# Performance work log

Measured on AMD Instinct MI355X. Metric: run time of the kernel, lower is better.

Reference implementation:

```python
import jax, jax.numpy as jnp
import numpy as np

DIM = 256
WH, WW = 7, 7
N = WH * WW
HEADS = 8
HEAD_DIM = DIM // HEADS
SCALE = HEAD_DIM ** -0.5
B_ = 4096
NW = 64  # windows per image; B_ % NW == 0


def _relative_position_index():
    coords = np.stack(np.meshgrid(np.arange(WH), np.arange(WW), indexing='ij'))  # (2,Wh,Ww)
    flat = coords.reshape(2, -1)  # (2,N)
    rel = flat[:, :, None] - flat[:, None, :]  # (2,N,N)
    rel = rel.transpose(1, 2, 0)  # (N,N,2)
    rel = rel + np.array([WH - 1, WW - 1])
    rel = rel * np.array([2 * WW - 1, 1])
    return rel.sum(-1).astype(np.int32)  # (N,N)


def setup_inputs() -> dict:
    key = jax.random.key(0)
    ks = jax.random.split(key, 7)
    num_rel = (2 * WH - 1) * (2 * WW - 1)
    return {
        'x': jax.random.normal(ks[0], (B_, N, DIM), jnp.float32),
        'mask': jax.random.normal(ks[1], (NW, N, N), jnp.float32),
        'qkv_w': jax.random.normal(ks[2], (DIM, 3 * DIM), jnp.float32) * 0.02,
        'qkv_b': jnp.zeros((3 * DIM,), jnp.float32),
        'proj_w': jax.random.normal(ks[3], (DIM, DIM), jnp.float32) * 0.02,
        'proj_b': jnp.zeros((DIM,), jnp.float32),
        'bias_table': jax.random.normal(ks[4], (num_rel, HEADS), jnp.float32) * 0.02,
        'rel_index': jnp.asarray(_relative_position_index()),
    }


def reference(x, mask, qkv_w, qkv_b, proj_w, proj_b, bias_table, rel_index):
    B, n, C = x.shape
    qkv = x @ qkv_w + qkv_b  # (B,N,3C)
    qkv = qkv.reshape(B, n, 3, HEADS, HEAD_DIM).transpose(2, 0, 3, 1, 4)
    q, k, v = qkv[0], qkv[1], qkv[2]  # (B,H,N,hd)
    attn = jnp.einsum('bhnd,bhmd->bhnm', q * SCALE, k)  # (B,H,N,N)
    rel_bias = bias_table[rel_index.reshape(-1)].reshape(n, n, HEADS)
    attn = attn + rel_bias.transpose(2, 0, 1)[None]  # (B,H,N,N)
    nW = mask.shape[0]
    attn = attn.reshape(-1, nW, HEADS, n, n) + mask[None, :, None]
    attn = attn.reshape(-1, HEADS, n, n)
    attn = jax.nn.softmax(attn, axis=-1)
    out = jnp.einsum('bhnm,bhmd->bhnd', attn, v)  # (B,H,N,hd)
    out = out.transpose(0, 2, 1, 3).reshape(B, n, C)
    return out @ proj_w + proj_b
```

## Files before the change

kernel.cpp:

```cpp
#include <hip/hip_runtime.h>
#include <hip/hip_bf16.h>


#define NTOK 49
static constexpr float SCALE_Q = 0.17677669529663687f;

using bf16   = __bf16;
using bf16x4 = __attribute__((ext_vector_type(4))) __bf16;
using bf16x8 = __attribute__((ext_vector_type(8))) __bf16;
using short4v = __attribute__((ext_vector_type(4))) short;
using f32x4  = __attribute__((ext_vector_type(4))) float;

#define WT_QKV_OFF 0
#define WT_PROJ_OFF (768 * 256 * 2)
#define SB_OFF (WT_PROJ_OFF + 256 * 256 * 2)
#define SM_OFF (SB_OFF + 8 * 4096 * 4)
#define WS_NEEDED (SM_OFF + (size_t)64 * 4096 * 4)

static __device__ __forceinline__ f32x4 mfma16(bf16x4 a, bf16x4 b, f32x4 c) {
#if __has_builtin(__builtin_amdgcn_mfma_f32_16x16x16_bf16)
    return __builtin_amdgcn_mfma_f32_16x16x16_bf16(a, b, c, 0, 0, 0);
#elif __has_builtin(__builtin_amdgcn_mfma_f32_16x16x16bf16_1k)
    return __builtin_amdgcn_mfma_f32_16x16x16bf16_1k(
        __builtin_bit_cast(short4v, a), __builtin_bit_cast(short4v, b), c, 0, 0, 0);
#elif __has_builtin(__builtin_amdgcn_mfma_f32_16x16x16_bf16_1k)
    return __builtin_amdgcn_mfma_f32_16x16x16_bf16_1k(
        __builtin_bit_cast(short4v, a), __builtin_bit_cast(short4v, b), c, 0, 0, 0);
#else
    asm volatile("v_mfma_f32_16x16x16_bf16 %0, %1, %2, %0\n\t"
                 "s_nop 7\n\ts_nop 7\n\ts_nop 1"
                 : "+v"(c) : "v"(a), "v"(b));
    return c;
#endif
}

__global__ void prep_wqkv(const float* __restrict__ qkv_w, bf16* __restrict__ wt) {
    int idx = blockIdx.x * 256 + threadIdx.x;
    if (idx >= 768 * 256) return;
    int n = idx >> 8, k = idx & 255;
    float v = qkv_w[k * 768 + n];
    if (n < 256) v *= SCALE_Q;
    wt[idx] = (bf16)v;
}
__global__ void prep_wproj(const float* __restrict__ proj_w, bf16* __restrict__ wt) {
    int idx = blockIdx.x * 256 + threadIdx.x;
    if (idx >= 256 * 256) return;
    int n = idx >> 8, k = idx & 255;
    wt[idx] = (bf16)proj_w[k * 256 + n];
}
__global__ void prep_sb(const float* __restrict__ bias_table, const int* __restrict__ rel_index,
                        float* __restrict__ sb) {
    int idx = blockIdx.x * 256 + threadIdx.x;
    if (idx >= 8 * 4096) return;
    int r    = idx & 3;
    int lane = (idx >> 2) & 63;
    int qp   = (idx >> 8) & 15;
    int h    = idx >> 12;
    int kt = qp >> 2, qt = qp & 3;
    int i = qt * 16 + (lane & 15);
    int j = kt * 16 + (lane >> 4) * 4 + r;
    float v;
    if (j >= NTOK)      v = -1e30f;
    else if (i >= NTOK) v = 0.0f;
    else v = bias_table[rel_index[i * 49 + j] * 8 + h];
    sb[idx] = v;
}
__global__ void prep_sm(const float* __restrict__ mask, float* __restrict__ sm) {
    int idx = blockIdx.x * 256 + threadIdx.x;
    if (idx >= 64 * 4096) return;
    int r    = idx & 3;
    int lane = (idx >> 2) & 63;
    int qp   = (idx >> 8) & 15;
    int w    = idx >> 12;
    int kt = qp >> 2, qt = qp & 3;
    int i = qt * 16 + (lane & 15);
    int j = kt * 16 + (lane >> 4) * 4 + r;
    sm[idx] = (i < NTOK && j < NTOK) ? mask[(w * 49 + i) * 49 + j] : 0.0f;
}

__global__ __launch_bounds__(512, 2) void fused_attn(
    const float* __restrict__ x,
    const float* __restrict__ qkv_b,
    const float* __restrict__ proj_b,
    const bf16* __restrict__ wt_qkv,
    const bf16* __restrict__ wt_proj,
    const float* __restrict__ sb,
    const float* __restrict__ sm,
    float* __restrict__ out)
{
    __shared__ char xs[32768];
    const int b    = blockIdx.x;
    const int tid  = threadIdx.x;
    const int lane = tid & 63;
    const int h    = tid >> 6;
    const int c    = lane & 15;
    const int g    = lane >> 4;

    {
        const float* xb = x + (size_t)b * (NTOK * 256);
        float4 xr[8];
        #pragma unroll
        for (int it = 0; it < 8; ++it) {
            int idx = it * 512 + tid;
            int row = idx >> 6, c4 = idx & 63;
            xr[it] = make_float4(0.f, 0.f, 0.f, 0.f);
            if (row < NTOK) xr[it] = ((const float4*)xb)[row * 64 + c4];
        }
        #pragma unroll
        for (int it = 0; it < 8; ++it) {
            int idx = it * 512 + tid;
            int row = idx >> 6, c4 = idx & 63;
            bf16x4 o;
            o[0] = (bf16)xr[it].x; o[1] = (bf16)xr[it].y;
            o[2] = (bf16)xr[it].z; o[3] = (bf16)xr[it].w;
            *(bf16x4*)(xs + row * 512 + ((c4 * 8) ^ ((row & 7) << 4))) = o;
        }
    }
    __syncthreads();

    bf16x4 iden;
    #pragma unroll
    for (int j = 0; j < 4; ++j) iden[j] = (bf16)((4 * g + j == c) ? 1.0f : 0.0f);

    bf16x4 qf[4][2];
    bf16x4 kf[4][2];
    bf16x4 pB[4][4];
    bf16x4 vf[2][4];
    bf16x4 ob[2][4];

    {
        f32x4 acc[2][4];
        #pragma unroll
        for (int ni = 0; ni < 2; ++ni)
            #pragma unroll
            for (int mi = 0; mi < 4; ++mi)
                acc[ni][mi] = (f32x4){0.f, 0.f, 0.f, 0.f};
        #pragma unroll
        for (int k2 = 0; k2 < 4; ++k2) {
            bf16x8 bb[2][2];
            #pragma unroll
            for (int ni = 0; ni < 2; ++ni)
                #pragma unroll
                for (int hf = 0; hf < 2; ++hf)
                    bb[ni][hf] = *(const bf16x8*)(wt_qkv + (h * 32 + ni * 16 + c) * 256
                                                  + k2 * 64 + hf * 32 + g * 8);
            bf16x8 a[2][4];
            #pragma unroll
            for (int hf = 0; hf < 2; ++hf)
                #pragma unroll
                for (int mi = 0; mi < 4; ++mi) {
                    int row = mi * 16 + c;
                    a[hf][mi] = *(const bf16x8*)(xs + row * 512
                                 + ((k2 * 128 + hf * 64 + g * 16) ^ ((row & 7) << 4)));
                }
            #pragma unroll
            for (int hf = 0; hf < 2; ++hf)
                #pragma unroll
                for (int ni = 0; ni < 2; ++ni)
                    #pragma unroll
                    for (int mi = 0; mi < 4; ++mi)
                        acc[ni][mi] = __builtin_amdgcn_mfma_f32_16x16x32_bf16(a[hf][mi], bb[ni][hf], acc[ni][mi], 0, 0, 0);
        }
        #pragma unroll
        for (int ni = 0; ni < 2; ++ni) {
            float bias = qkv_b[h * 32 + ni * 16 + c] * SCALE_Q;
            #pragma unroll
            for (int mi = 0; mi < 4; ++mi) {
                bf16x4 in;
                #pragma unroll
                for (int r = 0; r < 4; ++r) in[r] = (bf16)(acc[ni][mi][r] + bias);
                f32x4 t = mfma16(in, iden, (f32x4){0.f, 0.f, 0.f, 0.f});
                #pragma unroll
                for (int r = 0; r < 4; ++r) qf[mi][ni][r] = (bf16)t[r];
            }
        }
    }

    {
        f32x4 acc[2][4];
        #pragma unroll
        for (int ni = 0; ni < 2; ++ni)
            #pragma unroll
            for (int mi = 0; mi < 4; ++mi)
                acc[ni][mi] = (f32x4){0.f, 0.f, 0.f, 0.f};
        #pragma unroll
        for (int k2 = 0; k2 < 4; ++k2) {
            bf16x8 bb[2][2];
            #pragma unroll
            for (int ni = 0; ni < 2; ++ni)
                #pragma unroll
                for (int hf = 0; hf < 2; ++hf)
                    bb[ni][hf] = *(const bf16x8*)(wt_qkv + (256 + h * 32 + ni * 16 + c) * 256
                                                  + k2 * 64 + hf * 32 + g * 8);
            bf16x8 a[2][4];
            #pragma unroll
            for (int hf = 0; hf < 2; ++hf)
                #pragma unroll
                for (int mi = 0; mi < 4; ++mi) {
                    int row = mi * 16 + c;
                    a[hf][mi] = *(const bf16x8*)(xs + row * 512
                                 + ((k2 * 128 + hf * 64 + g * 16) ^ ((row & 7) << 4)));
                }
            #pragma unroll
            for (int hf = 0; hf < 2; ++hf)
                #pragma unroll
                for (int ni = 0; ni < 2; ++ni)
                    #pragma unroll
                    for (int mi = 0; mi < 4; ++mi)
                        acc[ni][mi] = __builtin_amdgcn_mfma_f32_16x16x32_bf16(a[hf][mi], bb[ni][hf], acc[ni][mi], 0, 0, 0);
        }
        #pragma unroll
        for (int ni = 0; ni < 2; ++ni) {
            float bias = qkv_b[256 + h * 32 + ni * 16 + c];
            #pragma unroll
            for (int mi = 0; mi < 4; ++mi) {
                bf16x4 in;
                #pragma unroll
                for (int r = 0; r < 4; ++r) in[r] = (bf16)(acc[ni][mi][r] + bias);
                f32x4 t = mfma16(in, iden, (f32x4){0.f, 0.f, 0.f, 0.f});
                #pragma unroll
                for (int r = 0; r < 4; ++r) kf[mi][ni][r] = (bf16)t[r];
            }
        }
    }

    {
        const float* sbh = sb + (size_t)h * 4096;
        const float* smw = sm + (size_t)(b & 63) * 4096;
        #pragma unroll
        for (int qt = 0; qt < 4; ++qt) {
            f32x4 sbv[4], smv[4];
            #pragma unroll
            for (int kt = 0; kt < 4; ++kt)
                sbv[kt] = *(const f32x4*)(sbh + (kt * 4 + qt) * 256 + lane * 4);
            #pragma unroll
            for (int kt = 0; kt < 4; ++kt)
                smv[kt] = *(const f32x4*)(smw + (kt * 4 + qt) * 256 + lane * 4);

            f32x4 sT[4];
            __builtin_amdgcn_s_setprio(1);
            #pragma unroll
            for (int kt = 0; kt < 4; ++kt) {
                sT[kt] = (f32x4){0.f, 0.f, 0.f, 0.f};
                sT[kt] = mfma16(kf[kt][0], qf[qt][0], sT[kt]);
                sT[kt] = mfma16(kf[kt][1], qf[qt][1], sT[kt]);
            }
            __builtin_amdgcn_s_setprio(0);
            #pragma unroll
            for (int kt = 0; kt < 4; ++kt)
                #pragma unroll
                for (int r = 0; r < 4; ++r)
                    sT[kt][r] += sbv[kt][r] + smv[kt][r];
            float m = sT[0][0];
            #pragma unroll
            for (int kt = 0; kt < 4; ++kt)
                #pragma unroll
                for (int r = 0; r < 4; ++r) m = fmaxf(m, sT[kt][r]);
            m = fmaxf(m, __shfl_xor(m, 16));
            m = fmaxf(m, __shfl_xor(m, 32));
            float sum = 0.f;
            #pragma unroll
            for (int kt = 0; kt < 4; ++kt)
                #pragma unroll
                for (int r = 0; r < 4; ++r) {
                    float e = __expf(sT[kt][r] - m);
                    sT[kt][r] = e;
                    sum += e;
                }
            sum += __shfl_xor(sum, 16);
            sum += __shfl_xor(sum, 32);
            float rs = 1.f / sum;
            #pragma unroll
            for (int kt = 0; kt < 4; ++kt)
                #pragma unroll
                for (int r = 0; r < 4; ++r) pB[qt][kt][r] = (bf16)(sT[kt][r] * rs);
        }
    }

    {
        f32x4 acc[2][4];
        #pragma unroll
        for (int dt = 0; dt < 2; ++dt)
            #pragma unroll
            for (int mi = 0; mi < 4; ++mi)
                acc[dt][mi] = (f32x4){0.f, 0.f, 0.f, 0.f};
        #pragma unroll
        for (int k2 = 0; k2 < 4; ++k2) {
            bf16x8 bb[2][2];
            #pragma unroll
            for (int dt = 0; dt < 2; ++dt)
                #pragma unroll
                for (int hf = 0; hf < 2; ++hf)
                    bb[dt][hf] = *(const bf16x8*)(wt_qkv + (512 + h * 32 + dt * 16 + c) * 256
                                                  + k2 * 64 + hf * 32 + g * 8);
            bf16x8 a[2][4];
            #pragma unroll
            for (int hf = 0; hf < 2; ++hf)
                #pragma unroll
                for (int mi = 0; mi < 4; ++mi) {
                    int row = mi * 16 + c;
                    a[hf][mi] = *(const bf16x8*)(xs + row * 512
                                 + ((k2 * 128 + hf * 64 + g * 16) ^ ((row & 7) << 4)));
                }
            #pragma unroll
            for (int hf = 0; hf < 2; ++hf)
                #pragma unroll
                for (int dt = 0; dt < 2; ++dt)
                    #pragma unroll
                    for (int mi = 0; mi < 4; ++mi)
                        acc[dt][mi] = __builtin_amdgcn_mfma_f32_16x16x32_bf16(a[hf][mi], bb[dt][hf], acc[dt][mi], 0, 0, 0);
        }
        #pragma unroll
        for (int dt = 0; dt < 2; ++dt) {
            float vb = qkv_b[512 + h * 32 + dt * 16 + c];
            #pragma unroll
            for (int kt = 0; kt < 4; ++kt)
                #pragma unroll
                for (int r = 0; r < 4; ++r) vf[dt][kt][r] = (bf16)(acc[dt][kt][r] + vb);
        }
    }

    __builtin_amdgcn_s_setprio(1);
    #pragma unroll
    for (int qt = 0; qt < 4; ++qt) {
        #pragma unroll
        for (int dt = 0; dt < 2; ++dt) {
            f32x4 oT = (f32x4){0.f, 0.f, 0.f, 0.f};
            #pragma unroll
            for (int kt = 0; kt < 4; ++kt)
                oT = mfma16(vf[dt][kt], pB[qt][kt], oT);
            #pragma unroll
            for (int r = 0; r < 4; ++r) ob[dt][qt][r] = (bf16)oT[r];
        }
    }
    __builtin_amdgcn_s_setprio(0);
    __syncthreads();

    #pragma unroll
    for (int qt = 0; qt < 4; ++qt) {
        int row = qt * 16 + c;
        #pragma unroll
        for (int dt = 0; dt < 2; ++dt) {
            int cbyte = h * 64 + dt * 32 + g * 8;
            *(bf16x4*)(xs + row * 512 + (cbyte ^ ((row & 7) << 4))) = ob[dt][qt];
        }
    }
    __syncthreads();

    {
        f32x4 po[2][4];
        #pragma unroll
        for (int ni = 0; ni < 2; ++ni)
            #pragma unroll
            for (int mi = 0; mi < 4; ++mi)
                po[ni][mi] = (f32x4){0.f, 0.f, 0.f, 0.f};

        #pragma unroll
        for (int k2 = 0; k2 < 4; ++k2) {
            bf16x8 bw[2][2];
            #pragma unroll
            for (int ni = 0; ni < 2; ++ni)
                #pragma unroll
                for (int hf = 0; hf < 2; ++hf)
                    bw[ni][hf] = *(const bf16x8*)(wt_proj + (h * 32 + ni * 16 + c) * 256
                                                  + k2 * 64 + hf * 32 + g * 8);
            bf16x8 a[2][4];
            #pragma unroll
            for (int hf = 0; hf < 2; ++hf)
                #pragma unroll
                for (int mi = 0; mi < 4; ++mi) {
                    int row = mi * 16 + c;
                    a[hf][mi] = *(const bf16x8*)(xs + row * 512
                                 + ((k2 * 128 + hf * 64 + g * 16) ^ ((row & 7) << 4)));
                }
            #pragma unroll
            for (int hf = 0; hf < 2; ++hf)
                #pragma unroll
                for (int ni = 0; ni < 2; ++ni)
                    #pragma unroll
                    for (int mi = 0; mi < 4; ++mi)
                        po[ni][mi] = __builtin_amdgcn_mfma_f32_16x16x32_bf16(a[hf][mi], bw[ni][hf], po[ni][mi], 0, 0, 0);
        }
        float* outb = out + (size_t)b * (NTOK * 256);
        #pragma unroll
        for (int ni = 0; ni < 2; ++ni) {
            int col = h * 32 + ni * 16 + c;
            float pb = proj_b[col];
            #pragma unroll
            for (int mi = 0; mi < 4; ++mi) {
                #pragma unroll
                for (int r = 0; r < 4; ++r) {
                    int row = mi * 16 + g * 4 + r;
                    if (row < NTOK) outb[row * 256 + col] = po[ni][mi][r] + pb;
                }
            }
        }
    }
}

extern "C" void kernel_launch(void* const* d_in, const int* in_sizes, int n_in,
                              void* d_out, int out_size, void* d_ws, size_t ws_size,
                              hipStream_t stream) {
    const float* x          = (const float*)d_in[0];
    const float* mask       = (const float*)d_in[1];
    const float* qkv_w      = (const float*)d_in[2];
    const float* qkv_b      = (const float*)d_in[3];
    const float* proj_w     = (const float*)d_in[4];
    const float* proj_b     = (const float*)d_in[5];
    const float* bias_table = (const float*)d_in[6];
    const int*   rel_index  = (const int*)d_in[7];
    float* out = (float*)d_out;

    if (ws_size < WS_NEEDED) return;

    char* ws = (char*)d_ws;
    bf16*  wt_qkv  = (bf16*)(ws + WT_QKV_OFF);
    bf16*  wt_proj = (bf16*)(ws + WT_PROJ_OFF);
    float* sbp     = (float*)(ws + SB_OFF);
    float* smp     = (float*)(ws + SM_OFF);

    prep_wqkv <<<768, 256, 0, stream>>>(qkv_w, wt_qkv);
    prep_wproj<<<256, 256, 0, stream>>>(proj_w, wt_proj);
    prep_sb   <<<128, 256, 0, stream>>>(bias_table, rel_index, sbp);
    prep_sm   <<<1024, 256, 0, stream>>>(mask, smp);

    fused_attn<<<4096, 512, 0, stream>>>(x, qkv_b, proj_b, wt_qkv, wt_proj, sbp, smp, out);
}
```

Measured before the change: 373.0 us.

## Cut register pressure to fit three blocks per CU in fused attention

Raises launch bounds from 2 to 3 blocks per multiprocessor and reshapes the QKV projection loops to load smaller register fragments per step (8 k-steps with 4 A-tiles instead of 4 with 8). The V projection is split per head-dim tile, the mask load is deferred until after the bias add, and the attention output is written straight to LDS instead of buffered in registers. The goal is to lower VGPR usage so more waves can overlap memory latency. The risk is register spilling under the tighter bound and fewer independent MFMAs in flight per step.

```diff
diff --git a/kernel.cpp b/kernel.cpp
--- a/kernel.cpp
+++ b/kernel.cpp
@@ -32,6 +32,10 @@
                  : "+v"(c) : "v"(a), "v"(b));
     return c;
 #endif
+}
+
+static __device__ __forceinline__ bf16x8 ldsA(const char* xs, int row, int koff) {
+    return *(const bf16x8*)(xs + row * 512 + (koff ^ ((row & 7) << 4)));
 }
 
 __global__ void prep_wqkv(const float* __restrict__ qkv_w, bf16* __restrict__ wt) {
@@ -78,7 +82,7 @@
     sm[idx] = (i < NTOK && j < NTOK) ? mask[(w * 49 + i) * 49 + j] : 0.0f;
 }
 
-__global__ __launch_bounds__(512, 2) void fused_attn(
+__global__ __launch_bounds__(512, 3) void fused_attn(
     const float* __restrict__ x,
     const float* __restrict__ qkv_b,
     const float* __restrict__ proj_b,
@@ -126,7 +130,6 @@
     bf16x4 kf[4][2];
     bf16x4 pB[4][4];
     bf16x4 vf[2][4];
-    bf16x4 ob[2][4];
 
     {
         f32x4 acc[2][4];
@@ -136,30 +139,20 @@
             for (int mi = 0; mi < 4; ++mi)
                 acc[ni][mi] = (f32x4){0.f, 0.f, 0.f, 0.f};
         #pragma unroll
-        for (int k2 = 0; k2 < 4; ++k2) {
-            bf16x8 bb[2][2];
-            #pragma unroll
-            for (int ni = 0; ni < 2; ++ni)
-                #pragma unroll
-                for (int hf = 0; hf < 2; ++hf)
-                    bb[ni][hf] = *(const bf16x8*)(wt_qkv + (h * 32 + ni * 16 + c) * 256
-                                                  + k2 * 64 + hf * 32 + g * 8);
-            bf16x8 a[2][4];
-            #pragma unroll
-            for (int hf = 0; hf < 2; ++hf)
-                #pragma unroll
-                for (int mi = 0; mi < 4; ++mi) {
-                    int row = mi * 16 + c;
-                    a[hf][mi] = *(const bf16x8*)(xs + row * 512
-                                 + ((k2 * 128 + hf * 64 + g * 16) ^ ((row & 7) << 4)));
-                }
-            #pragma unroll
-            for (int hf = 0; hf < 2; ++hf)
-                #pragma unroll
-                for (int ni = 0; ni < 2; ++ni)
-                    #pragma unroll
-                    for (int mi = 0; mi < 4; ++mi)
-                        acc[ni][mi] = __builtin_amdgcn_mfma_f32_16x16x32_bf16(a[hf][mi], bb[ni][hf], acc[ni][mi], 0, 0, 0);
+        for (int kk = 0; kk < 8; ++kk) {
+            bf16x8 bb[2];
+            #pragma unroll
+            for (int ni = 0; ni < 2; ++ni)
+                bb[ni] = *(const bf16x8*)(wt_qkv + (h * 32 + ni * 16 + c) * 256 + kk * 32 + g * 8);
+            bf16x8 a[4];
+            #pragma unroll
+            for (int mi = 0; mi < 4; ++mi)
+                a[mi] = ldsA(xs, mi * 16 + c, kk * 64 + g * 16);
+            #pragma unroll
+            for (int ni = 0; ni < 2; ++ni)
+                #pragma unroll
+                for (int mi = 0; mi < 4; ++mi)
+                    acc[ni][mi] = __builtin_amdgcn_mfma_f32_16x16x32_bf16(a[mi], bb[ni], acc[ni][mi], 0, 0, 0);
         }
         #pragma unroll
         for (int ni = 0; ni < 2; ++ni) {
@@ -184,30 +177,20 @@
             for (int mi = 0; mi < 4; ++mi)
                 acc[ni][mi] = (f32x4){0.f, 0.f, 0.f, 0.f};
         #pragma unroll
-        for (int k2 = 0; k2 < 4; ++k2) {
-            bf16x8 bb[2][2];
-            #pragma unroll
-            for (int ni = 0; ni < 2; ++ni)
-                #pragma unroll
-                for (int hf = 0; hf < 2; ++hf)
-                    bb[ni][hf] = *(const bf16x8*)(wt_qkv + (256 + h * 32 + ni * 16 + c) * 256
-                                                  + k2 * 64 + hf * 32 + g * 8);
-            bf16x8 a[2][4];
-            #pragma unroll
-            for (int hf = 0; hf < 2; ++hf)
-                #pragma unroll
-                for (int mi = 0; mi < 4; ++mi) {
-                    int row = mi * 16 + c;
-                    a[hf][mi] = *(const bf16x8*)(xs + row * 512
-                                 + ((k2 * 128 + hf * 64 + g * 16) ^ ((row & 7) << 4)));
-                }
-            #pragma unroll
-            for (int hf = 0; hf < 2; ++hf)
-                #pragma unroll
-                for (int ni = 0; ni < 2; ++ni)
-                    #pragma unroll
-                    for (int mi = 0; mi < 4; ++mi)
-                        acc[ni][mi] = __builtin_amdgcn_mfma_f32_16x16x32_bf16(a[hf][mi], bb[ni][hf], acc[ni][mi], 0, 0, 0);
+        for (int kk = 0; kk < 8; ++kk) {
+            bf16x8 bb[2];
+            #pragma unroll
+            for (int ni = 0; ni < 2; ++ni)
+                bb[ni] = *(const bf16x8*)(wt_qkv + (256 + h * 32 + ni * 16 + c) * 256 + kk * 32 + g * 8);
+            bf16x8 a[4];
+            #pragma unroll
+            for (int mi = 0; mi < 4; ++mi)
+                a[mi] = ldsA(xs, mi * 16 + c, kk * 64 + g * 16);
+            #pragma unroll
+            for (int ni = 0; ni < 2; ++ni)
+                #pragma unroll
+                for (int mi = 0; mi < 4; ++mi)
+                    acc[ni][mi] = __builtin_amdgcn_mfma_f32_16x16x32_bf16(a[mi], bb[ni], acc[ni][mi], 0, 0, 0);
         }
         #pragma unroll
         for (int ni = 0; ni < 2; ++ni) {
@@ -229,13 +212,10 @@
         const float* smw = sm + (size_t)(b & 63) * 4096;
         #pragma unroll
         for (int qt = 0; qt < 4; ++qt) {
-            f32x4 sbv[4], smv[4];
+            f32x4 sbv[4];
             #pragma unroll
             for (int kt = 0; kt < 4; ++kt)
                 sbv[kt] = *(const f32x4*)(sbh + (kt * 4 + qt) * 256 + lane * 4);
-            #pragma unroll
-            for (int kt = 0; kt < 4; ++kt)
-                smv[kt] = *(const f32x4*)(smw + (kt * 4 + qt) * 256 + lane * 4);
 
             f32x4 sT[4];
             __builtin_amdgcn_s_setprio(1);
@@ -250,7 +230,16 @@
             for (int kt = 0; kt < 4; ++kt)
                 #pragma unroll
                 for (int r = 0; r < 4; ++r)
-                    sT[kt][r] += sbv[kt][r] + smv[kt][r];
+                    sT[kt][r] += sbv[kt][r];
+            f32x4 smv[4];
+            #pragma unroll
+            for (int kt = 0; kt < 4; ++kt)
+                smv[kt] = *(const f32x4*)(smw + (kt * 4 + qt) * 256 + lane * 4);
+            #pragma unroll
+            for (int kt = 0; kt < 4; ++kt)
+                #pragma unroll
+                for (int r = 0; r < 4; ++r)
+                    sT[kt][r] += smv[kt][r];
             float m = sT[0][0];
             #pragma unroll
             for (int kt = 0; kt < 4; ++kt)
@@ -277,74 +266,49 @@
         }
     }
 
-    {
-        f32x4 acc[2][4];
-        #pragma unroll
-        for (int dt = 0; dt < 2; ++dt)
-            #pragma unroll
-            for (int mi = 0; mi < 4; ++mi)
-                acc[dt][mi] = (f32x4){0.f, 0.f, 0.f, 0.f};
-        #pragma unroll
-        for (int k2 = 0; k2 < 4; ++k2) {
-            bf16x8 bb[2][2];
-            #pragma unroll
-            for (int dt = 0; dt < 2; ++dt)
-                #pragma unroll
-                for (int hf = 0; hf < 2; ++hf)
-                    bb[dt][hf] = *(const bf16x8*)(wt_qkv + (512 + h * 32 + dt * 16 + c) * 256
-                                                  + k2 * 64 + hf * 32 + g * 8);
-            bf16x8 a[2][4];
-            #pragma unroll
-            for (int hf = 0; hf < 2; ++hf)
-                #pragma unroll
-                for (int mi = 0; mi < 4; ++mi) {
-                    int row = mi * 16 + c;
-                    a[hf][mi] = *(const bf16x8*)(xs + row * 512
-                                 + ((k2 * 128 + hf * 64 + g * 16) ^ ((row & 7) << 4)));
-                }
-            #pragma unroll
-            for (int hf = 0; hf < 2; ++hf)
-                #pragma unroll
-                for (int dt = 0; dt < 2; ++dt)
-                    #pragma unroll
-                    for (int mi = 0; mi < 4; ++mi)
-                        acc[dt][mi] = __builtin_amdgcn_mfma_f32_16x16x32_bf16(a[hf][mi], bb[dt][hf], acc[dt][mi], 0, 0, 0);
-        }
-        #pragma unroll
-        for (int dt = 0; dt < 2; ++dt) {
-            float vb = qkv_b[512 + h * 32 + dt * 16 + c];
-            #pragma unroll
-            for (int kt = 0; kt < 4; ++kt)
-                #pragma unroll
-                for (int r = 0; r < 4; ++r) vf[dt][kt][r] = (bf16)(acc[dt][kt][r] + vb);
-        }
-    }
+    #pragma unroll
+    for (int dt = 0; dt < 2; ++dt) {
+        f32x4 acc[4];
+        #pragma unroll
+        for (int mi = 0; mi < 4; ++mi)
+            acc[mi] = (f32x4){0.f, 0.f, 0.f, 0.f};
+        #pragma unroll
+        for (int kk = 0; kk < 8; ++kk) {
+            bf16x8 bv = *(const bf16x8*)(wt_qkv + (512 + h * 32 + dt * 16 + c) * 256 + kk * 32 + g * 8);
+            bf16x8 a[4];
+            #pragma unroll
+            for (int mi = 0; mi < 4; ++mi)
+                a[mi] = ldsA(xs, mi * 16 + c, kk * 64 + g * 16);
+            #pragma unroll
+            for (int mi = 0; mi < 4; ++mi)
+                acc[mi] = __builtin_amdgcn_mfma_f32_16x16x32_bf16(a[mi], bv, acc[mi], 0, 0, 0);
+        }
+        float vb = qkv_b[512 + h * 32 + dt * 16 + c];
+        #pragma unroll
+        for (int kt = 0; kt < 4; ++kt)
+            #pragma unroll
+            for (int r = 0; r < 4; ++r) vf[dt][kt][r] = (bf16)(acc[kt][r] + vb);
+    }
+    __syncthreads();
 
     __builtin_amdgcn_s_setprio(1);
     #pragma unroll
     for (int qt = 0; qt < 4; ++qt) {
+        int row = qt * 16 + c;
         #pragma unroll
         for (int dt = 0; dt < 2; ++dt) {
             f32x4 oT = (f32x4){0.f, 0.f, 0.f, 0.f};
             #pragma unroll
             for (int kt = 0; kt < 4; ++kt)
                 oT = mfma16(vf[dt][kt], pB[qt][kt], oT);
-            #pragma unroll
-            for (int r = 0; r < 4; ++r) ob[dt][qt][r] = (bf16)oT[r];
+            int cbyte = h * 64 + dt * 32 + g * 8;
+            bf16x4 o;
+            #pragma unroll
+            for (int r = 0; r < 4; ++r) o[r] = (bf16)oT[r];
+            *(bf16x4*)(xs + row * 512 + (cbyte ^ ((row & 7) << 4))) = o;
         }
     }
     __builtin_amdgcn_s_setprio(0);
-    __syncthreads();
-
-    #pragma unroll
-    for (int qt = 0; qt < 4; ++qt) {
-        int row = qt * 16 + c;
-        #pragma unroll
-        for (int dt = 0; dt < 2; ++dt) {
-            int cbyte = h * 64 + dt * 32 + g * 8;
-            *(bf16x4*)(xs + row * 512 + (cbyte ^ ((row & 7) << 4))) = ob[dt][qt];
-        }
-    }
     __syncthreads();
 
     {
@@ -368,11 +332,8 @@
             #pragma unroll
             for (int hf = 0; hf < 2; ++hf)
                 #pragma unroll
-                for (int mi = 0; mi < 4; ++mi) {
-                    int row = mi * 16 + c;
-                    a[hf][mi] = *(const bf16x8*)(xs + row * 512
-                                 + ((k2 * 128 + hf * 64 + g * 16) ^ ((row & 7) << 4)));
-                }
+                for (int mi = 0; mi < 4; ++mi)
+                    a[hf][mi] = ldsA(xs, mi * 16 + c, k2 * 128 + hf * 64 + g * 16);
             #pragma unroll
             for (int hf = 0; hf < 2; ++hf)
                 #pragma unroll
```

After: 376.6 us. About the same (+1.0%).
